# Performance work log

Hardware: AMD Instinct MI355X
Metric: run time of the kernel (lower is better)

The kernel has to match this reference:

```python
import jax, jax.numpy as jnp
import numpy as np

B, ACT, DICT = 4096, 768, 12288
TOP_K_AUX = 512
N_DEAD = 1024
AUX_PENALTY = 0.03125
SOFTMAX_AUX_PENALTY = 0.01
L1_COEFF = 0.001  # fraction=1 >= l1_warmup_frac -> full coeff
EPS = 1e-5


def setup_inputs() -> dict:
    key = jax.random.key(0)
    k1, k2, k3 = jax.random.split(key, 3)
    x = jax.random.normal(k1, (B, ACT), dtype=jnp.float32)
    # kaiming-uniform-scale init for W_enc, W_dec = normalized W_enc.T (as in __init__)
    bound = np.sqrt(6.0 / ACT)
    W_enc = jax.random.uniform(k2, (ACT, DICT), dtype=jnp.float32, minval=-bound, maxval=bound)
    W_dec = W_enc.T
    W_dec = W_dec / jnp.linalg.norm(W_dec, axis=-1, keepdims=True)
    b_enc = jnp.zeros((DICT,), dtype=jnp.float32)
    b_dec = jnp.zeros((ACT,), dtype=jnp.float32)
    quantile_threshold = jnp.full((1,), 0.1, dtype=jnp.float32)
    dead_features = jnp.zeros((DICT,), dtype=bool).at[:N_DEAD].set(True)
    return {"x": x, "W_enc": W_enc, "W_dec": W_dec, "b_enc": b_enc,
            "b_dec": b_dec, "quantile_threshold": quantile_threshold,
            "dead_features": dead_features}


def reference(x, W_enc, W_dec, b_enc, b_dec, quantile_threshold, dead_features):
    # input unit-norm (torch .std uses ddof=1)
    x_mean = jnp.mean(x, axis=-1, keepdims=True)
    x = x - x_mean
    x_std = jnp.std(x, axis=-1, keepdims=True, ddof=1)
    x = x / (x_std + EPS)

    x_cent = x - b_dec
    acts_pre = x_cent @ W_enc + b_enc          # [B, DICT]
    acts = jax.nn.relu(acts_pre)

    acts_mask = acts > quantile_threshold
    acts_thresholded = acts * acts_mask
    x_reconstruct = acts_thresholded @ W_dec + b_dec  # [B, ACT]

    residual = x - x_reconstruct

    # aux path 1: topk over dead features only (dead count >= TOP_K_AUX by setup)
    neg_inf = jnp.asarray(-jnp.inf, dtype=acts.dtype)
    masked_acts = jnp.where(dead_features, acts, neg_inf)
    vals, idx = jax.lax.top_k(masked_acts, TOP_K_AUX)  # [B, K]
    rows = jnp.arange(B)[:, None]
    acts_aux = jnp.zeros_like(acts).at[rows, idx].set(vals)  # nonzero only on dead cols
    x_reconstruct_aux = acts_aux @ W_dec + b_dec
    l2_loss_aux = AUX_PENALTY * jnp.mean((x_reconstruct_aux - residual) ** 2)

    # aux path 2: softmax-weighted pre-activations over dead features
    acts_softmax_aux = acts_pre * jax.nn.softmax(acts_pre, axis=-1) * 64.0
    x_reconstruct_softmax = (acts_softmax_aux * dead_features) @ W_dec + b_dec
    l2_loss_softmax = SOFTMAX_AUX_PENALTY * jnp.mean((x_reconstruct_softmax - residual) ** 2)

    l2_loss = jnp.mean((x_reconstruct - x) ** 2)
    l1_norm = jnp.mean(jnp.sum(jnp.abs(acts_thresholded), axis=-1))
    l1_loss = L1_COEFF * l1_norm
    l0_norm = jnp.mean(jnp.sum((acts_thresholded > 0).astype(jnp.float32), axis=-1))

    loss = l2_loss + l1_loss + l2_loss_aux + l2_loss_softmax

    # final rescale (as written in source: * x_std + x, with x the normalized input)
    sae_out = x_reconstruct * x_std + x
    num_dead = jnp.sum(dead_features.astype(jnp.int32))
    return (sae_out, acts_thresholded, loss, l2_loss, l1_loss, l0_norm,
            l1_norm, l2_loss_aux, l2_loss_softmax, num_dead)
```

## Files before the change

### kernel.cpp

```cpp
#include <hip/hip_runtime.h>

#define B_    4096
#define ACT   768
#define DICT  12288
#define KTOP  512
#define NDMAX 1024
#define AUX_PEN  0.03125f
#define SOFT_PEN 0.01f
#define L1_CO    0.001f
#define EPS_     1e-5f
#define NBLK_FE  1536
#define PLANE    (B_ * ACT)
#define SPLITK2  4
#define SPLITK3  2

typedef __attribute__((ext_vector_type(4))) float f32x4;
typedef __attribute__((ext_vector_type(4))) unsigned int u32x4;
typedef __attribute__((ext_vector_type(8))) short short8;
typedef __attribute__((ext_vector_type(8))) __bf16 bf8_t;

__device__ __forceinline__ float b2f(unsigned short u) {
    return __uint_as_float(((unsigned)u) << 16);
}
__device__ __forceinline__ unsigned short f2b(float f) {
    unsigned u = __float_as_uint(f);
    unsigned r = (u + 0x7FFFu + ((u >> 16) & 1u)) >> 16;
    return (unsigned short)r;
}
__device__ __forceinline__ unsigned cvtpk_bf16(float lo, float hi) {
    unsigned r;
    asm("v_cvt_pk_bf16_f32 %0, %1, %2" : "=v"(r) : "v"(lo), "v"(hi));
    return r;
}

__device__ __forceinline__ float wredsum(float v) {
#pragma unroll
    for (int o = 32; o; o >>= 1) v += __shfl_down(v, o);
    return v;
}
__device__ __forceinline__ float wredmax(float v) {
#pragma unroll
    for (int o = 32; o; o >>= 1) v = fmaxf(v, __shfl_down(v, o));
    return v;
}
__device__ __forceinline__ int wredsumi(int v) {
#pragma unroll
    for (int o = 32; o; o >>= 1) v += __shfl_down(v, o);
    return v;
}
__device__ __forceinline__ float bredsum(float v, float* sh) {
    int lane = threadIdx.x & 63, w = threadIdx.x >> 6;
    v = wredsum(v);
    __syncthreads();
    if (!lane) sh[w] = v;
    __syncthreads();
    return sh[0] + sh[1] + sh[2] + sh[3];
}
__device__ __forceinline__ float bredmax(float v, float* sh) {
    int lane = threadIdx.x & 63, w = threadIdx.x >> 6;
    v = wredmax(v);
    __syncthreads();
    if (!lane) sh[w] = v;
    __syncthreads();
    return fmaxf(fmaxf(sh[0], sh[1]), fmaxf(sh[2], sh[3]));
}
__device__ __forceinline__ int bredsumi(int v, int* sh) {
    int lane = threadIdx.x & 63, w = threadIdx.x >> 6;
    v = wredsumi(v);
    __syncthreads();
    if (!lane) sh[w] = v;
    __syncthreads();
    return sh[0] + sh[1] + sh[2] + sh[3];
}

__device__ __forceinline__ void gload16(const void* g, const void* lds_base) {
    __builtin_amdgcn_global_load_lds((const __attribute__((address_space(1))) void*)g,
                                     (__attribute__((address_space(3))) void*)lds_base,
                                     16, 0, 0);
}

__global__ __launch_bounds__(256) void norm_kernel(
    const float* __restrict__ x, float* __restrict__ xn,
    unsigned short* __restrict__ xnb, float* __restrict__ xstd)
{
    __shared__ float sh[4];
    const int row = blockIdx.x, t = threadIdx.x;
    const float* xr = x + (size_t)row * ACT;
    float v0 = xr[t], v1 = xr[t + 256], v2 = xr[t + 512];
    float s = bredsum(v0 + v1 + v2, sh);
    float mean = s * (1.0f / ACT);
    v0 -= mean; v1 -= mean; v2 -= mean;
    float s2 = bredsum(v0 * v0 + v1 * v1 + v2 * v2, sh);
    float sd = sqrtf(s2 / (float)(ACT - 1));
    float inv = 1.0f / (sd + EPS_);
    v0 *= inv; v1 *= inv; v2 *= inv;
    size_t base = (size_t)row * ACT;
    xn[base + t] = v0; xn[base + t + 256] = v1; xn[base + t + 512] = v2;
    xnb[base + t] = f2b(v0); xnb[base + t + 256] = f2b(v1); xnb[base + t + 512] = f2b(v2);
    if (!t) xstd[row] = sd;
}

__global__ __launch_bounds__(256) void transpose_bf16(
    const float* __restrict__ in, unsigned short* __restrict__ out, int R, int C)
{
    __shared__ float tile[64][65];
    const int c0 = blockIdx.x * 64, r0 = blockIdx.y * 64;
    const int t = threadIdx.x;
#pragma unroll
    for (int i = 0; i < 16; i++) {
        int lin = t + i * 256;
        int r = lin >> 6, c = lin & 63;
        tile[r][c] = in[(size_t)(r0 + r) * C + c0 + c];
    }
    __syncthreads();
#pragma unroll
    for (int i = 0; i < 16; i++) {
        int lin = t + i * 256;
        int cc = lin >> 6, rr = lin & 63;
        out[(size_t)(c0 + cc) * R + r0 + rr] = f2b(tile[rr][cc]);
    }
}

__global__ __launch_bounds__(256) void cvec_kernel(
    const float* __restrict__ benc, const float* __restrict__ bdec,
    const float* __restrict__ wenc, float* __restrict__ cvec)
{
    int j = blockIdx.x * 256 + threadIdx.x;
    float acc = 0.f;
    for (int k = 0; k < ACT; k++) acc += bdec[k] * wenc[(size_t)k * DICT + j];
    cvec[j] = benc[j] - acc;
}

__global__ __launch_bounds__(256) void dead_scan(
    const void* __restrict__ dead_raw, int* __restrict__ dead_list, int* __restrict__ ndp)
{
    __shared__ int cnt[256];
    const unsigned char* u8 = (const unsigned char*)dead_raw;
    const unsigned* u32p = (const unsigned*)dead_raw;
    unsigned w0 = u32p[0];
    int mode;
    if (w0 == 0x01010101u) mode = 1;
    else if (w0 == 0x3F800000u) mode = 2;
    else if (w0 == 1u) mode = 0;
    else mode = (u8[1] | u8[2] | u8[3]) ? 1 : 0;

    const int t = threadIdx.x;
    const int per = DICT / 256;
    const int base = t * per;
    int c = 0;
    for (int i = 0; i < per; i++) {
        int j = base + i;
        bool d = (mode == 1) ? (u8[j] != 0)
               : (mode == 2) ? (((const float*)dead_raw)[j] != 0.f)
                             : (((const int*)dead_raw)[j] != 0);
        c += d ? 1 : 0;
    }
    cnt[t] = c;
    __syncthreads();
    if (!t) {
        int run = 0;
        for (int i = 0; i < 256; i++) { int v = cnt[i]; cnt[i] = run; run += v; }
        *ndp = run;
    }
    __syncthreads();
    int o = cnt[t];
    for (int i = 0; i < per; i++) {
        int j = base + i;
        bool d = (mode == 1) ? (u8[j] != 0)
               : (mode == 2) ? (((const float*)dead_raw)[j] != 0.f)
                             : (((const int*)dead_raw)[j] != 0);
        if (d) dead_list[o++] = j;
    }
}

__global__ __launch_bounds__(256) void gemm1_kernel(
    const unsigned short* __restrict__ A, const unsigned short* __restrict__ Bt,
    const float* __restrict__ cvec, const float* __restrict__ qtp,
    unsigned short* __restrict__ actspre, float* __restrict__ out_thr)
{
    __shared__ __align__(16) unsigned short As[2][128 * 32];
    __shared__ __align__(16) unsigned short Bs[2][128 * 32];
    const int tid = threadIdx.x, lane = tid & 63, wave = tid >> 6;
    const int wr = wave >> 1, wc = wave & 1;
    const int lr = lane & 15, lg = lane >> 4;
    const int row0 = blockIdx.x * 128, col0 = blockIdx.y * 128;
    const int nsteps = ACT / 32;
    f32x4 acc[4][4] = {};

    auto stage = [&](int kt, int b) {
#pragma unroll
        for (int i = 0; i < 2; i++) {
            int c = wave * 2 + i;
            int o = c * 1024;
            int ol = o + lane * 16;
            int r = ol >> 6;
            int cb = (ol & 63) ^ (((r >> 1) & 3) << 4);
            gload16((const char*)A + (size_t)(row0 + r) * (ACT * 2) + kt * 2 + cb,
                    (const char*)As[b] + o);
            gload16((const char*)Bt + (size_t)(col0 + r) * (ACT * 2) + kt * 2 + cb,
                    (const char*)Bs[b] + o);
        }
    };

    stage(0, 0);
    __syncthreads();
    int cur = 0;
    for (int t = 0; t < nsteps; ++t) {
        const int nxt = cur ^ 1;
        if (t + 1 < nsteps) stage((t + 1) * 32, nxt);
        bf8_t af[4], bfr[4];
#pragma unroll
        for (int m = 0; m < 4; m++) {
            int row = wr * 64 + m * 16 + lr;
            af[m] = *(const bf8_t*)((const char*)As[cur] + row * 64 + ((lg * 16) ^ (((row >> 1) & 3) << 4)));
        }
#pragma unroll
        for (int n = 0; n < 4; n++) {
            int col = wc * 64 + n * 16 + lr;
            bfr[n] = *(const bf8_t*)((const char*)Bs[cur] + col * 64 + ((lg * 16) ^ (((col >> 1) & 3) << 4)));
        }
#pragma unroll
        for (int m = 0; m < 4; m++)
#pragma unroll
            for (int n = 0; n < 4; n++)
                acc[m][n] = __builtin_amdgcn_mfma_f32_16x16x32_bf16(af[m], bfr[n], acc[m][n], 0, 0, 0);
        __syncthreads();
        cur = nxt;
    }
    const float qt = fmaxf(qtp[0], 0.0f);
#pragma unroll
    for (int m = 0; m < 4; m++) {
        int row = row0 + wr * 64 + m * 16 + lg * 4;
#pragma unroll
        for (int n = 0; n < 4; n++) {
            int col = col0 + wc * 64 + n * 16 + lr;
            float cadd = cvec[col];
#pragma unroll
            for (int r = 0; r < 4; r++) {
                float v = acc[m][n][r] + cadd;
                size_t idx = (size_t)(row + r) * DICT + col;
                actspre[idx] = f2b(v);
                float a = fmaxf(v, 0.f);
                out_thr[idx] = (a > qt) ? a : 0.f;
            }
        }
    }
}

__global__ __launch_bounds__(256) void softrow_kernel(
    const unsigned short* __restrict__ actspre, const float* __restrict__ qtp,
    const int* __restrict__ dead_list, const int* __restrict__ ndp,
    unsigned short* __restrict__ asoft, unsigned short* __restrict__ aaux,
    float* __restrict__ l1row, float* __restrict__ l0row)
{
    __shared__ __align__(16) unsigned short rowv[DICT];
    __shared__ float shf[4];
    __shared__ int shi[4];
    const int t = threadIdx.x, row = blockIdx.x;
    const unsigned short* src = actspre + (size_t)row * DICT;
    short8 v[6];
    float mx = -1e30f;
#pragma unroll
    for (int i = 0; i < 6; i++) {
        v[i] = *(const short8*)(src + i * 2048 + t * 8);
        *(short8*)(rowv + i * 2048 + t * 8) = v[i];
#pragma unroll
        for (int e = 0; e < 8; e++) mx = fmaxf(mx, b2f((unsigned short)v[i][e]));
    }
    mx = bredmax(mx, shf);
    const float qt = fmaxf(qtp[0], 0.0f);
    float se = 0.f, l1 = 0.f, l0 = 0.f;
#pragma unroll
    for (int i = 0; i < 6; i++)
#pragma unroll
        for (int e = 0; e < 8; e++) {
            float f = b2f((unsigned short)v[i][e]);
            se += __expf(f - mx);
            float a = fmaxf(f, 0.f);
            float tv = (a > qt) ? a : 0.f;
            l1 += tv;
            l0 += (tv > 0.f) ? 1.f : 0.f;
        }
    se = bredsum(se, shf);
    l1 = bredsum(l1, shf);
    l0 = bredsum(l0, shf);
    if (!t) { l1row[row] = l1; l0row[row] = l0; }

    float inv64 = 64.0f / se;
    int nd = *ndp; if (nd > NDMAX) nd = NDMAX;
    unsigned keys[4]; float av_[4];
#pragma unroll
    for (int i = 0; i < 4; i++) {
        int k = t + i * 256;
        float f = 0.f;
        if (k < nd) {
            int idx = dead_list[k];
            f = b2f(rowv[idx]);
            asoft[(size_t)row * NDMAX + k] = f2b(f * __expf(f - mx) * inv64);
        } else {
            asoft[(size_t)row * NDMAX + k] = 0;
        }
        float a = (k < nd) ? fmaxf(f, 0.f) : 0.f;
        av_[i] = a;
        keys[i] = __float_as_uint(a);
    }
    unsigned lo = 0u, hi = 0x7F800000u;
    while (hi - lo > 1u) {
        unsigned mid = lo + ((hi - lo) >> 1);
        int c = 0;
#pragma unroll
        for (int i = 0; i < 4; i++) c += (keys[i] >= mid) ? 1 : 0;
        c = bredsumi(c, shi);
        if (c >= KTOP) lo = mid; else hi = mid;
    }
#pragma unroll
    for (int i = 0; i < 4; i++) {
        int k = t + i * 256;
        aaux[(size_t)row * NDMAX + k] = f2b((keys[i] >= lo) ? av_[i] : 0.f);
    }
}

__global__ __launch_bounds__(256) void wdead_gather(
    const unsigned short* __restrict__ wdec_t, const int* __restrict__ dead_list,
    const int* __restrict__ ndp, unsigned short* __restrict__ wdead)
{
    int n = blockIdx.x;
    int nd = *ndp; if (nd > NDMAX) nd = NDMAX;
    for (int k = threadIdx.x; k < NDMAX; k += 256)
        wdead[(size_t)n * NDMAX + k] = (k < nd) ? wdec_t[(size_t)n * DICT + dead_list[k]] : 0;
}

__global__ __launch_bounds__(256) void gemm2_kernel(
    const float* __restrict__ Athr, const unsigned short* __restrict__ Bt,
    float* __restrict__ pxr)
{
    __shared__ __align__(16) unsigned short As[2][128 * 32];
    __shared__ __align__(16) unsigned short Bs[2][128 * 32];
    const int tid = threadIdx.x, lane = tid & 63, wave = tid >> 6;
    const int wr = wave >> 1, wc = wave & 1;
    const int lr = lane & 15, lg = lane >> 4;
    const int flat = blockIdx.x;
    const int xcd = flat & 7, s = flat >> 3;
    const int q = s / 6, m_ = s - 6 * q;
    const int g = q * 8 + xcd;
    const int col0 = m_ * 128;
    const int row0 = (g & 31) * 128;
    const int zidx = g >> 5;
    const int kbase = zidx * (DICT / SPLITK2);
    const int nsteps = (DICT / SPLITK2) / 32;
    const int ar = tid >> 1, ah = tid & 1;
    const int aswz = ((ar >> 1) & 3) << 4;
    f32x4 acc[4][4] = {};

    auto stageB = [&](int kt, int b) {
#pragma unroll
        for (int i = 0; i < 2; i++) {
            int c = wave * 2 + i;
            int o = c * 1024;
            int ol = o + lane * 16;
            int r = ol >> 6;
            int cb = (ol & 63) ^ (((r >> 1) & 3) << 4);
            gload16((const char*)Bt + (size_t)(col0 + r) * (DICT * 2) + (size_t)kt * 2 + cb,
                    (const char*)Bs[b] + o);
        }
    };
    auto writeA = [&](const f32x4& fv0, const f32x4& fv1, const f32x4& fv2, const f32x4& fv3, int b) {
        u32x4 w0 = { cvtpk_bf16(fv0.x, fv0.y), cvtpk_bf16(fv0.z, fv0.w),
                     cvtpk_bf16(fv1.x, fv1.y), cvtpk_bf16(fv1.z, fv1.w) };
        u32x4 w1 = { cvtpk_bf16(fv2.x, fv2.y), cvtpk_bf16(fv2.z, fv2.w),
                     cvtpk_bf16(fv3.x, fv3.y), cvtpk_bf16(fv3.z, fv3.w) };
        *(u32x4*)((char*)As[b] + ar * 64 + ((ah * 32 +  0) ^ aswz)) = w0;
        *(u32x4*)((char*)As[b] + ar * 64 + ((ah * 32 + 16) ^ aswz)) = w1;
    };

    {
        const float* gsrc = Athr + (size_t)(row0 + ar) * DICT + kbase + ah * 16;
        f32x4 p0 = ((const f32x4*)gsrc)[0];
        f32x4 p1 = ((const f32x4*)gsrc)[1];
        f32x4 p2 = ((const f32x4*)gsrc)[2];
        f32x4 p3 = ((const f32x4*)gsrc)[3];
        stageB(kbase, 0);
        writeA(p0, p1, p2, p3, 0);
    }
    __syncthreads();

    int cur = 0;
    for (int t = 0; t < nsteps; ++t) {
        const int nxt = cur ^ 1;
        const bool pf = (t + 1 < nsteps);
        f32x4 p0, p1, p2, p3;
        if (pf) {
            const int kt = kbase + (t + 1) * 32;
            const float* gsrc = Athr + (size_t)(row0 + ar) * DICT + kt + ah * 16;
            p0 = ((const f32x4*)gsrc)[0];
            p1 = ((const f32x4*)gsrc)[1];
            p2 = ((const f32x4*)gsrc)[2];
            p3 = ((const f32x4*)gsrc)[3];
            stageB(kt, nxt);
        }
        bf8_t af[4], bfr[4];
#pragma unroll
        for (int m = 0; m < 4; m++) {
            int row = wr * 64 + m * 16 + lr;
            af[m] = *(const bf8_t*)((const char*)As[cur] + row * 64 + ((lg * 16) ^ (((row >> 1) & 3) << 4)));
        }
#pragma unroll
        for (int n = 0; n < 4; n++) {
            int col = wc * 64 + n * 16 + lr;
            bfr[n] = *(const bf8_t*)((const char*)Bs[cur] + col * 64 + ((lg * 16) ^ (((col >> 1) & 3) << 4)));
        }
#pragma unroll
        for (int m = 0; m < 4; m++)
#pragma unroll
            for (int n = 0; n < 4; n++)
                acc[m][n] = __builtin_amdgcn_mfma_f32_16x16x32_bf16(af[m], bfr[n], acc[m][n], 0, 0, 0);
        if (pf) writeA(p0, p1, p2, p3, nxt);
        __syncthreads();
        cur = nxt;
    }
    float* out = pxr + (size_t)zidx * PLANE;
#pragma unroll
    for (int m = 0; m < 4; m++) {
        int row = row0 + wr * 64 + m * 16 + lg * 4;
#pragma unroll
        for (int n = 0; n < 4; n++) {
            int col = col0 + wc * 64 + n * 16 + lr;
#pragma unroll
            for (int r = 0; r < 4; r++)
                out[(size_t)(row + r) * ACT + col] = acc[m][n][r];
        }
    }
}

__global__ __launch_bounds__(256) void gemm3_kernel(
    const unsigned short* __restrict__ A1, const unsigned short* __restrict__ A2,
    const unsigned short* __restrict__ Bt,
    float* __restrict__ praux, float* __restrict__ prsoft)
{
    __shared__ __align__(16) unsigned short A1s[128 * 64];
    __shared__ __align__(16) unsigned short A2s[128 * 64];
    __shared__ __align__(16) unsigned short Bs[128 * 64];
    const int tid = threadIdx.x, lane = tid & 63, wave = tid >> 6;
    const int wr = wave >> 1, wc = wave & 1;
    const int lr = lane & 15, lg = lane >> 4;
    const int flat = blockIdx.x;
    const int xcd = flat & 7, s = flat >> 3;
    const int q = s / 6, m_ = s - 6 * q;
    const int g = q * 8 + xcd;
    const int col0 = m_ * 128;
    const int row0 = (g & 31) * 128;
    const int zidx = g >> 5;
    const int kbase = zidx * (NDMAX / SPLITK3);
    const int kend  = kbase + (NDMAX / SPLITK3);
    f32x4 acc1[4][4] = {}, acc2[4][4] = {};

    for (int kt = kbase; kt < kend; kt += 64) {
#pragma unroll
        for (int i = 0; i < 4; i++) {
            int chunk = wave * 4 + i;
            int o = chunk * 1024;
            int ol = o + lane * 16;
            int r = ol >> 7;
            int b = (ol & 127) ^ ((r & 7) << 4);
            gload16((const char*)A1 + (size_t)(row0 + r) * (NDMAX * 2) + kt * 2 + b, (const char*)A1s + o);
            gload16((const char*)A2 + (size_t)(row0 + r) * (NDMAX * 2) + kt * 2 + b, (const char*)A2s + o);
            gload16((const char*)Bt + (size_t)(col0 + r) * (NDMAX * 2) + kt * 2 + b, (const char*)Bs + o);
        }
        __syncthreads();
#pragma unroll
        for (int kk = 0; kk < 64; kk += 32) {
            bf8_t a1f[4], a2f[4], bfr[4];
#pragma unroll
            for (int m = 0; m < 4; m++) {
                int row = wr * 64 + m * 16 + lr;
                int bo = (kk * 2 + lg * 16) ^ ((row & 7) << 4);
                a1f[m] = *(const bf8_t*)((const char*)A1s + row * 128 + bo);
                a2f[m] = *(const bf8_t*)((const char*)A2s + row * 128 + bo);
            }
#pragma unroll
            for (int n = 0; n < 4; n++) {
                int col = wc * 64 + n * 16 + lr;
                bfr[n] = *(const bf8_t*)((const char*)Bs + col * 128 + ((kk * 2 + lg * 16) ^ ((col & 7) << 4)));
            }
#pragma unroll
            for (int m = 0; m < 4; m++)
#pragma unroll
                for (int n = 0; n < 4; n++) {
                    acc1[m][n] = __builtin_amdgcn_mfma_f32_16x16x32_bf16(a1f[m], bfr[n], acc1[m][n], 0, 0, 0);
                    acc2[m][n] = __builtin_amdgcn_mfma_f32_16x16x32_bf16(a2f[m], bfr[n], acc2[m][n], 0, 0, 0);
                }
        }
        __syncthreads();
    }
    float* o1 = praux  + (size_t)zidx * PLANE;
    float* o2 = prsoft + (size_t)zidx * PLANE;
#pragma unroll
    for (int m = 0; m < 4; m++) {
        int row = row0 + wr * 64 + m * 16 + lg * 4;
#pragma unroll
        for (int n = 0; n < 4; n++) {
            int col = col0 + wc * 64 + n * 16 + lr;
#pragma unroll
            for (int r = 0; r < 4; r++) {
                size_t idx = (size_t)(row + r) * ACT + col;
                o1[idx] = acc1[m][n][r];
                o2[idx] = acc2[m][n][r];
            }
        }
    }
}

__global__ __launch_bounds__(256) void final_elem(
    const float* __restrict__ pxr, const float* __restrict__ praux,
    const float* __restrict__ prsoft, const float* __restrict__ xn,
    const float* __restrict__ xstd, const float* __restrict__ bdec,
    float* __restrict__ sae_out, float* __restrict__ partials)
{
    __shared__ float sh[4];
    const int t = threadIdx.x, blk = blockIdx.x;
    const int base = blk * 2048;
    float s2 = 0.f, sa = 0.f, ss = 0.f;
#pragma unroll
    for (int i = 0; i < 8; i++) {
        int idx = base + t + i * 256;
        int row = idx / ACT;
        int col = idx - row * ACT;
        float bd = bdec[col];
        float r  = pxr[idx] + pxr[PLANE + idx] + pxr[2 * PLANE + idx] + pxr[3 * PLANE + idx] + bd;
        float ra = praux[idx] + praux[PLANE + idx] + bd;
        float rs = prsoft[idx] + prsoft[PLANE + idx] + bd;
        float xv = xn[idx];
        float resid = xv - r;
        float da = ra - resid;
        float dsf = rs - resid;
        s2 += resid * resid;
        sa += da * da;
        ss += dsf * dsf;
        sae_out[idx] = r * xstd[row] + xv;
    }
    s2 = bredsum(s2, sh);
    sa = bredsum(sa, sh);
    ss = bredsum(ss, sh);
    if (!t) {
        partials[blk] = s2;
        partials[NBLK_FE + blk] = sa;
        partials[2 * NBLK_FE + blk] = ss;
    }
}

__global__ __launch_bounds__(256) void final_scalar(
    const float* __restrict__ partials, const float* __restrict__ l1row,
    const float* __restrict__ l0row, const int* __restrict__ ndp,
    float* __restrict__ out_sc)
{
    __shared__ float sh[4];
    const int t = threadIdx.x;
    float s2 = 0.f, sa = 0.f, ss = 0.f;
    for (int i = t; i < NBLK_FE; i += 256) {
        s2 += partials[i];
        sa += partials[NBLK_FE + i];
        ss += partials[2 * NBLK_FE + i];
    }
    s2 = bredsum(s2, sh);
    sa = bredsum(sa, sh);
    ss = bredsum(ss, sh);
    float l1 = 0.f, l0 = 0.f;
    for (int i = t; i < B_; i += 256) { l1 += l1row[i]; l0 += l0row[i]; }
    l1 = bredsum(l1, sh);
    l0 = bredsum(l0, sh);
    if (!t) {
        const float n = (float)B_ * (float)ACT;
        float l2   = s2 / n;
        float l2a  = AUX_PEN  * (sa / n);
        float l2s  = SOFT_PEN * (ss / n);
        float l1n  = l1 / (float)B_;
        float l1l  = L1_CO * l1n;
        float l0n  = l0 / (float)B_;
        float loss = l2 + l1l + l2a + l2s;
        out_sc[0] = loss;
        out_sc[1] = l2;
        out_sc[2] = l1l;
        out_sc[3] = l0n;
        out_sc[4] = l1n;
        out_sc[5] = l2a;
        out_sc[6] = l2s;
        out_sc[7] = (float)(*ndp);
    }
}

extern "C" void kernel_launch(void* const* d_in, const int* in_sizes, int n_in,
                              void* d_out, int out_size, void* d_ws, size_t ws_size,
                              hipStream_t stream)
{
    const float* x    = (const float*)d_in[0];
    const float* Wenc = (const float*)d_in[1];
    const float* Wdec = (const float*)d_in[2];
    const float* benc = (const float*)d_in[3];
    const float* bdec = (const float*)d_in[4];
    const float* qtp  = (const float*)d_in[5];
    const void*  dead = d_in[6];

    float* out_sae = (float*)d_out;
    float* out_thr = out_sae + (size_t)B_ * ACT;
    float* out_sc  = out_thr + (size_t)B_ * DICT;

    char* w = (char*)d_ws;
    auto alloc = [&](size_t bytes) -> char* {
        char* p = w;
        w += (bytes + 255) & ~(size_t)255;
        return p;
    };
    float*          xn      = (float*)alloc((size_t)B_ * ACT * 4);
    unsigned short* xnb     = (unsigned short*)alloc((size_t)B_ * ACT * 2);
    float*          xstd    = (float*)alloc((size_t)B_ * 4);
    unsigned short* wenc_t  = (unsigned short*)alloc((size_t)DICT * ACT * 2);
    unsigned short* wdec_t  = (unsigned short*)alloc((size_t)ACT * DICT * 2);
    float*          cvec    = (float*)alloc((size_t)DICT * 4);
    unsigned short* actspre = (unsigned short*)alloc((size_t)B_ * DICT * 2);
    unsigned short* asoft   = (unsigned short*)alloc((size_t)B_ * NDMAX * 2);
    unsigned short* aaux    = (unsigned short*)alloc((size_t)B_ * NDMAX * 2);
    unsigned short* wdead   = (unsigned short*)alloc((size_t)ACT * NDMAX * 2);
    float*          l1row   = (float*)alloc((size_t)B_ * 4);
    float*          l0row   = (float*)alloc((size_t)B_ * 4);
    float*          partials= (float*)alloc((size_t)3 * NBLK_FE * 4);
    int*            dlist   = (int*)alloc((size_t)DICT * 4);
    int*            ndp     = (int*)alloc(256);

    float* pxr    = (float*)actspre;
    float* praux  = pxr + (size_t)SPLITK2 * PLANE;
    float* prsoft = praux + (size_t)SPLITK3 * PLANE;

    norm_kernel<<<B_, 256, 0, stream>>>(x, xn, xnb, xstd);
    transpose_bf16<<<dim3(DICT / 64, ACT / 64), 256, 0, stream>>>(Wenc, wenc_t, ACT, DICT);
    transpose_bf16<<<dim3(ACT / 64, DICT / 64), 256, 0, stream>>>(Wdec, wdec_t, DICT, ACT);
    cvec_kernel<<<DICT / 256, 256, 0, stream>>>(benc, bdec, Wenc, cvec);
    dead_scan<<<1, 256, 0, stream>>>(dead, dlist, ndp);
    gemm1_kernel<<<dim3(B_ / 128, DICT / 128), 256, 0, stream>>>(xnb, wenc_t, cvec, qtp, actspre, out_thr);
    softrow_kernel<<<B_, 256, 0, stream>>>(actspre, qtp, dlist, ndp, asoft, aaux, l1row, l0row);
    wdead_gather<<<ACT, 256, 0, stream>>>(wdec_t, dlist, ndp, wdead);
    gemm2_kernel<<<768, 256, 0, stream>>>(out_thr, wdec_t, pxr);
    gemm3_kernel<<<384, 256, 0, stream>>>(aaux, asoft, wdead, praux, prsoft);
    final_elem<<<NBLK_FE, 256, 0, stream>>>(pxr, praux, prsoft, xn, xstd, bdec, out_sae, partials);
    final_scalar<<<1, 256, 0, stream>>>(partials, l1row, l0row, ndp, out_sc);
}
```

Baseline: 578.0 us.

## Feed decoder GEMM from bf16 pre-activations with on-the-fly thresholding

The decoder GEMM now reads the bf16 pre-activation buffer through async global-to-LDS loads and applies relu and the quantile threshold while loading MFMA fragments. Before, it read the fp32 thresholded output and converted it to bf16 in registers. This halves the A-operand traffic and removes the register-staged conversion path. Because actspre is still live, the split-K partials are moved into the xnb buffer and a new allocation, with final_elem updated to read both. The risk is that xnb may be too small to hold two fp32 planes, which would overlap other buffers, and the per-fragment compare adds ALU work in the inner loop.

```diff
diff --git a/kernel.cpp b/kernel.cpp
--- a/kernel.cpp
+++ b/kernel.cpp
@@ -27,10 +27,16 @@
     unsigned r = (u + 0x7FFFu + ((u >> 16) & 1u)) >> 16;
     return (unsigned short)r;
 }
-__device__ __forceinline__ unsigned cvtpk_bf16(float lo, float hi) {
-    unsigned r;
-    asm("v_cvt_pk_bf16_f32 %0, %1, %2" : "=v"(r) : "v"(lo), "v"(hi));
-    return r;
+
+__device__ __forceinline__ bf8_t thr8(bf8_t v, float qt) {
+    union { bf8_t b; unsigned short u[8]; } x;
+    x.b = v;
+#pragma unroll
+    for (int e = 0; e < 8; e++) {
+        float f = b2f(x.u[e]);
+        x.u[e] = (f > qt) ? x.u[e] : (unsigned short)0;
+    }
+    return x.b;
 }
 
 __device__ __forceinline__ float wredsum(float v) {
@@ -331,8 +337,8 @@
 }
 
 __global__ __launch_bounds__(256) void gemm2_kernel(
-    const float* __restrict__ Athr, const unsigned short* __restrict__ Bt,
-    float* __restrict__ pxr)
+    const unsigned short* __restrict__ Apre, const unsigned short* __restrict__ Bt,
+    const float* __restrict__ qtp, float* __restrict__ pxrA, float* __restrict__ pxrB)
 {
     __shared__ __align__(16) unsigned short As[2][128 * 32];
     __shared__ __align__(16) unsigned short Bs[2][128 * 32];
@@ -348,11 +354,10 @@
     const int zidx = g >> 5;
     const int kbase = zidx * (DICT / SPLITK2);
     const int nsteps = (DICT / SPLITK2) / 32;
-    const int ar = tid >> 1, ah = tid & 1;
-    const int aswz = ((ar >> 1) & 3) << 4;
+    const float qt = fmaxf(qtp[0], 0.0f);
     f32x4 acc[4][4] = {};
 
-    auto stageB = [&](int kt, int b) {
+    auto stage = [&](int kt, int b) {
 #pragma unroll
         for (int i = 0; i < 2; i++) {
             int c = wave * 2 + i;
@@ -360,49 +365,24 @@
             int ol = o + lane * 16;
             int r = ol >> 6;
             int cb = (ol & 63) ^ (((r >> 1) & 3) << 4);
+            gload16((const char*)Apre + (size_t)(row0 + r) * (DICT * 2) + (size_t)kt * 2 + cb,
+                    (const char*)As[b] + o);
             gload16((const char*)Bt + (size_t)(col0 + r) * (DICT * 2) + (size_t)kt * 2 + cb,
                     (const char*)Bs[b] + o);
         }
     };
-    auto writeA = [&](const f32x4& fv0, const f32x4& fv1, const f32x4& fv2, const f32x4& fv3, int b) {
-        u32x4 w0 = { cvtpk_bf16(fv0.x, fv0.y), cvtpk_bf16(fv0.z, fv0.w),
-                     cvtpk_bf16(fv1.x, fv1.y), cvtpk_bf16(fv1.z, fv1.w) };
-        u32x4 w1 = { cvtpk_bf16(fv2.x, fv2.y), cvtpk_bf16(fv2.z, fv2.w),
-                     cvtpk_bf16(fv3.x, fv3.y), cvtpk_bf16(fv3.z, fv3.w) };
-        *(u32x4*)((char*)As[b] + ar * 64 + ((ah * 32 +  0) ^ aswz)) = w0;
-        *(u32x4*)((char*)As[b] + ar * 64 + ((ah * 32 + 16) ^ aswz)) = w1;
-    };
-
-    {
-        const float* gsrc = Athr + (size_t)(row0 + ar) * DICT + kbase + ah * 16;
-        f32x4 p0 = ((const f32x4*)gsrc)[0];
-        f32x4 p1 = ((const f32x4*)gsrc)[1];
-        f32x4 p2 = ((const f32x4*)gsrc)[2];
-        f32x4 p3 = ((const f32x4*)gsrc)[3];
-        stageB(kbase, 0);
-        writeA(p0, p1, p2, p3, 0);
-    }
-    __syncthreads();
-
+
+    stage(kbase, 0);
+    __syncthreads();
     int cur = 0;
     for (int t = 0; t < nsteps; ++t) {
         const int nxt = cur ^ 1;
-        const bool pf = (t + 1 < nsteps);
-        f32x4 p0, p1, p2, p3;
-        if (pf) {
-            const int kt = kbase + (t + 1) * 32;
-            const float* gsrc = Athr + (size_t)(row0 + ar) * DICT + kt + ah * 16;
-            p0 = ((const f32x4*)gsrc)[0];
-            p1 = ((const f32x4*)gsrc)[1];
-            p2 = ((const f32x4*)gsrc)[2];
-            p3 = ((const f32x4*)gsrc)[3];
-            stageB(kt, nxt);
-        }
+        if (t + 1 < nsteps) stage(kbase + (t + 1) * 32, nxt);
         bf8_t af[4], bfr[4];
 #pragma unroll
         for (int m = 0; m < 4; m++) {
             int row = wr * 64 + m * 16 + lr;
-            af[m] = *(const bf8_t*)((const char*)As[cur] + row * 64 + ((lg * 16) ^ (((row >> 1) & 3) << 4)));
+            af[m] = thr8(*(const bf8_t*)((const char*)As[cur] + row * 64 + ((lg * 16) ^ (((row >> 1) & 3) << 4))), qt);
         }
 #pragma unroll
         for (int n = 0; n < 4; n++) {
@@ -414,11 +394,11 @@
 #pragma unroll
             for (int n = 0; n < 4; n++)
                 acc[m][n] = __builtin_amdgcn_mfma_f32_16x16x32_bf16(af[m], bfr[n], acc[m][n], 0, 0, 0);
-        if (pf) writeA(p0, p1, p2, p3, nxt);
         __syncthreads();
         cur = nxt;
     }
-    float* out = pxr + (size_t)zidx * PLANE;
+    float* out = (zidx < 2) ? (pxrA + (size_t)zidx * PLANE)
+                            : (pxrB + (size_t)(zidx - 2) * PLANE);
 #pragma unroll
     for (int m = 0; m < 4; m++) {
         int row = row0 + wr * 64 + m * 16 + lg * 4;
@@ -511,9 +491,10 @@
 }
 
 __global__ __launch_bounds__(256) void final_elem(
-    const float* __restrict__ pxr, const float* __restrict__ praux,
-    const float* __restrict__ prsoft, const float* __restrict__ xn,
-    const float* __restrict__ xstd, const float* __restrict__ bdec,
+    const float* __restrict__ pxrA, const float* __restrict__ pxrB,
+    const float* __restrict__ praux, const float* __restrict__ prsoft,
+    const float* __restrict__ xn, const float* __restrict__ xstd,
+    const float* __restrict__ bdec,
     float* __restrict__ sae_out, float* __restrict__ partials)
 {
     __shared__ float sh[4];
@@ -526,7 +507,7 @@
         int row = idx / ACT;
         int col = idx - row * ACT;
         float bd = bdec[col];
-        float r  = pxr[idx] + pxr[PLANE + idx] + pxr[2 * PLANE + idx] + pxr[3 * PLANE + idx] + bd;
+        float r  = pxrA[idx] + pxrA[PLANE + idx] + pxrB[idx] + pxrB[PLANE + idx] + bd;
         float ra = praux[idx] + praux[PLANE + idx] + bd;
         float rs = prsoft[idx] + prsoft[PLANE + idx] + bd;
         float xv = xn[idx];
@@ -612,7 +593,6 @@
     };
     float*          xn      = (float*)alloc((size_t)B_ * ACT * 4);
     unsigned short* xnb     = (unsigned short*)alloc((size_t)B_ * ACT * 2);
-    float*          xstd    = (float*)alloc((size_t)B_ * 4);
     unsigned short* wenc_t  = (unsigned short*)alloc((size_t)DICT * ACT * 2);
     unsigned short* wdec_t  = (unsigned short*)alloc((size_t)ACT * DICT * 2);
     float*          cvec    = (float*)alloc((size_t)DICT * 4);
@@ -620,14 +600,16 @@
     unsigned short* asoft   = (unsigned short*)alloc((size_t)B_ * NDMAX * 2);
     unsigned short* aaux    = (unsigned short*)alloc((size_t)B_ * NDMAX * 2);
     unsigned short* wdead   = (unsigned short*)alloc((size_t)ACT * NDMAX * 2);
+    float*          xstd    = (float*)alloc((size_t)B_ * 4);
     float*          l1row   = (float*)alloc((size_t)B_ * 4);
     float*          l0row   = (float*)alloc((size_t)B_ * 4);
     float*          partials= (float*)alloc((size_t)3 * NBLK_FE * 4);
     int*            dlist   = (int*)alloc((size_t)DICT * 4);
     int*            ndp     = (int*)alloc(256);
-
-    float* pxr    = (float*)actspre;
-    float* praux  = pxr + (size_t)SPLITK2 * PLANE;
+    float*          pxrB    = (float*)alloc((size_t)2 * PLANE * 4);
+
+    float* pxrA = (float*)xnb;
+    float* praux  = (float*)actspre;
     float* prsoft = praux + (size_t)SPLITK3 * PLANE;
 
     norm_kernel<<<B_, 256, 0, stream>>>(x, xn, xnb, xstd);
@@ -638,8 +620,8 @@
     gemm1_kernel<<<dim3(B_ / 128, DICT / 128), 256, 0, stream>>>(xnb, wenc_t, cvec, qtp, actspre, out_thr);
     softrow_kernel<<<B_, 256, 0, stream>>>(actspre, qtp, dlist, ndp, asoft, aaux, l1row, l0row);
     wdead_gather<<<ACT, 256, 0, stream>>>(wdec_t, dlist, ndp, wdead);
-    gemm2_kernel<<<768, 256, 0, stream>>>(out_thr, wdec_t, pxr);
+    gemm2_kernel<<<768, 256, 0, stream>>>(actspre, wdec_t, qtp, pxrA, pxrB);
     gemm3_kernel<<<384, 256, 0, stream>>>(aaux, asoft, wdead, praux, prsoft);
-    final_elem<<<NBLK_FE, 256, 0, stream>>>(pxr, praux, prsoft, xn, xstd, bdec, out_sae, partials);
+    final_elem<<<NBLK_FE, 256, 0, stream>>>(pxrA, pxrB, praux, prsoft, xn, xstd, bdec, out_sae, partials);
     final_scalar<<<1, 256, 0, stream>>>(partials, l1row, l0row, ndp, out_sc);
 }
```

Result: slower. 597.0 us (+3.3%).
